# Optimization experiments

Hardware: AMD Instinct MI355X
Metric: run time of the kernel (lower is better)

## Reference

```python
import jax, jax.numpy as jnp
import numpy as np

MARGIN = 1.0
NUM_CLASSES = 1024


def setup_inputs() -> dict:
    key = jax.random.key(0)
    k1, k2 = jax.random.split(key)
    embeddings = jax.random.normal(k1, (8192, 128), dtype=jnp.float32)
    labels = jax.random.randint(k2, (8192,), 0, NUM_CLASSES, dtype=jnp.int64)
    return {"embeddings": embeddings, "labels": labels}


def reference(embeddings, labels):
    """Triplet loss with hard-negative mining, fully vectorized.

    Matches TripletLossWithMining(margin=1.0, mining_strategy='hard'):
      - squared-Euclidean pairwise distance matrix, relu-clamped, zero diagonal
      - for every (anchor i, positive p): hardest negative n* = argmin_{n: label!=label_i} d[i,n]
      - triplet kept iff d[i,n*] < d[i,p]; loss = mean relu(d[i,p] - d[i,n*] + margin)
    """
    B = embeddings.shape[0]
    sq = jnp.sum(embeddings * embeddings, axis=1, keepdims=True)          # [B,1]
    dist = sq + sq.T - 2.0 * (embeddings @ embeddings.T)                   # [B,B]
    dist = jax.nn.relu(dist)
    eye = jnp.eye(B, dtype=bool)
    dist = jnp.where(eye, jnp.zeros((), dist.dtype), dist)                 # fill_diagonal_(0)

    same = labels[:, None] == labels[None, :]                              # [B,B]
    pos_mask = same & ~eye
    neg_mask = ~same
    has_neg = jnp.any(neg_mask, axis=1)                                    # [B]

    # hardest (closest) negative per anchor
    neg_d = jnp.where(neg_mask, dist, jnp.array(jnp.inf, dist.dtype))
    hardest_neg = jnp.min(neg_d, axis=1)                                   # [B]

    # triplet (i,p) is kept iff p is a valid positive, i has a negative,
    # and hardest_neg[i] < pos_dist d[i,p]
    valid = pos_mask & has_neg[:, None] & (hardest_neg[:, None] < dist)    # [B,B]

    per_triplet = jax.nn.relu(dist - hardest_neg[:, None] + MARGIN)        # [B,B]
    count = jnp.sum(valid)
    total = jnp.sum(jnp.where(valid, per_triplet, jnp.zeros((), dist.dtype)))
    loss = total / jnp.maximum(count, 1).astype(dist.dtype)
    return loss, count
```

## Files before the change

kernel.cpp:

```cpp
#include <hip/hip_runtime.h>
#include <stdint.h>

#define BB 8192
#define DD 128
#define MARGIN 1.0f
#define CCAP 48
#define NBLK_POS (BB / 4)
#define NCH 16
#define CHCOLS (BB / NCH)
#define TPC (CHCOLS / 64)

typedef __attribute__((ext_vector_type(8))) short short8_t;
typedef __attribute__((ext_vector_type(4))) float f32x4;

#define GLL16(g, l)                                                                   \
  __builtin_amdgcn_global_load_lds(                                                   \
      (const __attribute__((address_space(1))) unsigned int*)(g),                     \
      (__attribute__((address_space(3))) unsigned int*)(l), 16, 0, 0)

__device__ __forceinline__ unsigned short f2bf(float f) {
  unsigned u = __float_as_uint(f);
  u = (u + 0x7fffu + ((u >> 16) & 1u)) >> 16;
  return (unsigned short)u;
}

__global__ void prep_kernel(const float* __restrict__ E, const int* __restrict__ lab,
                            unsigned short* __restrict__ Ebf,
                            float* __restrict__ sq,
                            int* __restrict__ cls_cnt, int* __restrict__ cls_idx) {
  int wid = threadIdx.x >> 6, lane = threadIdx.x & 63;
  int row = blockIdx.x * 4 + wid;
  const float2 v = *(const float2*)(E + (size_t)row * DD + lane * 2);
  ushort2 bb;
  bb.x = f2bf(v.x);
  bb.y = f2bf(v.y);
  *(ushort2*)(Ebf + (size_t)row * DD + lane * 2) = bb;
  float s = v.x * v.x + v.y * v.y;
  for (int off = 1; off < 64; off <<= 1) s += __shfl_xor(s, off);
  if (lane == 0) {
    sq[row] = s;
    int labi = lab[row];
    int p = atomicAdd(&cls_cnt[labi], 1);
    if (p < CCAP) cls_idx[labi * CCAP + p] = row;
  }
}

__global__ __launch_bounds__(256, 3) void dist_min_kernel(
    const unsigned short* __restrict__ Ebf, const float* __restrict__ sq,
    const int* __restrict__ lab, float* __restrict__ part) {
  __shared__ __align__(16) char ldsB[2][64 * 256];
  __shared__ int labC[CHCOLS];
  __shared__ float hC[CHCOLS];
  __shared__ int labI[128];
  __shared__ float redMin[4][64];

  const int tid = threadIdx.x;
  const int p = blockIdx.x >> 4, c = blockIdx.x & (NCH - 1);
  const int rI = p * 128;
  const int cBase = c * CHCOLS;

  const int wid = tid >> 6, lane = tid & 63;
  const int l4 = lane >> 4, c16 = lane & 15;
  const int wr = wid >> 1, wc = wid & 1;
  const int rowbase = wr * 64;
  const int cl = c16, rg = l4;

  short8_t a[4][4];
#pragma unroll
  for (int m = 0; m < 4; m++) {
    const char* rowp = (const char*)Ebf + (size_t)(rI + rowbase + m * 16 + cl) * 256 + rg * 16;
#pragma unroll
    for (int kk = 0; kk < 4; kk++) a[m][kk] = *(const short8_t*)(rowp + kk * 64);
  }

#pragma unroll
  for (int q = 0; q < 4; q++) {
    int r = wid * 16 + q * 4 + l4;
    int chunk = c16 ^ (r & 7);
    GLL16((const char*)Ebf + (size_t)(cBase + r) * 256 + chunk * 16,
          ldsB[0] + wid * 4096 + q * 1024);
  }
  for (int q = tid; q < CHCOLS; q += 256) {
    labC[q] = lab[cBase + q];
    hC[q] = 0.5f * sq[cBase + q];
  }
  if (tid < 128) labI[tid] = lab[rI + tid];
  __syncthreads();

  int il[4][4];
#pragma unroll
  for (int m = 0; m < 4; m++)
#pragma unroll
    for (int r = 0; r < 4; r++) il[m][r] = labI[rowbase + m * 16 + rg * 4 + r];

  float tm[4][4];
#pragma unroll
  for (int m = 0; m < 4; m++)
#pragma unroll
    for (int r = 0; r < 4; r++) tm[m][r] = __builtin_huge_valf();

  for (int t = 0; t < TPC; t++) {
    const int cur = t & 1;
    if (t + 1 < TPC) {
#pragma unroll
      for (int q = 0; q < 4; q++) {
        int r = wid * 16 + q * 4 + l4;
        int chunk = c16 ^ (r & 7);
        GLL16((const char*)Ebf + (size_t)(cBase + (t + 1) * 64 + r) * 256 + chunk * 16,
              ldsB[cur ^ 1] + wid * 4096 + q * 1024);
      }
    }

    int jl[2];
    float jh[2];
#pragma unroll
    for (int n = 0; n < 2; n++) {
      int j = t * 64 + wc * 32 + n * 16 + cl;
      jl[n] = labC[j];
      jh[n] = hC[j];
    }

    f32x4 acc[4][2];
#pragma unroll
    for (int m = 0; m < 4; m++)
#pragma unroll
      for (int n = 0; n < 2; n++) acc[m][n] = (f32x4){0.f, 0.f, 0.f, 0.f};

#pragma unroll
    for (int kk = 0; kk < 4; kk++) {
      const int kb = kk * 64 + rg * 16;
      short8_t b[2];
#pragma unroll
      for (int n = 0; n < 2; n++) {
        int row = wc * 32 + n * 16 + cl;
        b[n] = *(const short8_t*)(ldsB[cur] + row * 256 + (kb ^ ((row & 7) << 4)));
      }
#pragma unroll
      for (int m = 0; m < 4; m++)
#pragma unroll
        for (int n = 0; n < 2; n++)
          acc[m][n] = __builtin_amdgcn_mfma_f32_16x16x32_bf16(a[m][kk], b[n], acc[m][n], 0, 0, 0);
    }

#pragma unroll
    for (int m = 0; m < 4; m++)
#pragma unroll
      for (int n = 0; n < 2; n++) {
        f32x4 v = acc[m][n];
#pragma unroll
        for (int r = 0; r < 4; r++) {
          float u = jh[n] - v[r];
          if (il[m][r] != jl[n]) tm[m][r] = fminf(tm[m][r], u);
        }
      }

    __syncthreads();
  }

#pragma unroll
  for (int m = 0; m < 4; m++)
#pragma unroll
    for (int r = 0; r < 4; r++) {
      float t = tm[m][r];
      t = fminf(t, __shfl_xor(t, 1));
      t = fminf(t, __shfl_xor(t, 2));
      t = fminf(t, __shfl_xor(t, 4));
      t = fminf(t, __shfl_xor(t, 8));
      tm[m][r] = t;
    }
  if (cl == 0) {
#pragma unroll
    for (int m = 0; m < 4; m++)
#pragma unroll
      for (int r = 0; r < 4; r++) redMin[wid][m * 16 + rg * 4 + r] = tm[m][r];
  }
  __syncthreads();
  if (wc == 0) {
    float v = fminf(redMin[wid][lane], redMin[wid + 1][lane]);
    part[(size_t)c * BB + rI + rowbase + lane] = v;
  }
}

__global__ void pos_loss_kernel(const float* __restrict__ E, const int* __restrict__ lab,
                                const float* __restrict__ sq, const float* __restrict__ part,
                                const int* __restrict__ cls_cnt, const int* __restrict__ cls_idx,
                                float* __restrict__ ptot, int* __restrict__ pcnt) {
  __shared__ float stot[4];
  __shared__ int scnt[4];
  const int tid = threadIdx.x, wid = tid >> 6, lane = tid & 63;
  const int i = blockIdx.x * 4 + wid;
  const int labi = lab[i];
  int n = cls_cnt[labi];
  if (n > CCAP) n = CCAP;
  const float2 ei = *(const float2*)(E + (size_t)i * DD + lane * 2);
  const float sqi = sq[i];
  float mn = __builtin_huge_valf();
#pragma unroll
  for (int cc = 0; cc < NCH; cc++) mn = fminf(mn, part[(size_t)cc * BB + i]);
  const float hn = fmaxf(sqi + 2.0f * mn, 0.0f);
  float tsum = 0.0f;
  int tcnt = 0;
  for (int s = 0; s < n; s++) {
    int j = cls_idx[labi * CCAP + s];
    if (j == i) continue;
    float2 ej = *(const float2*)(E + (size_t)j * DD + lane * 2);
    float pp = ei.x * ej.x + ei.y * ej.y;
    for (int off = 1; off < 64; off <<= 1) pp += __shfl_xor(pp, off);
    float d = fmaxf(sqi + sq[j] - 2.0f * pp, 0.0f);
    if (hn < d) {
      tcnt++;
      tsum += d - hn + MARGIN;
    }
  }
  if (lane == 0) {
    stot[wid] = tsum;
    scnt[wid] = tcnt;
  }
  __syncthreads();
  if (tid == 0) {
    ptot[blockIdx.x] = stot[0] + stot[1] + stot[2] + stot[3];
    pcnt[blockIdx.x] = scnt[0] + scnt[1] + scnt[2] + scnt[3];
  }
}

__global__ void finalize_kernel(const float* __restrict__ ptot, const int* __restrict__ pcnt,
                                float* __restrict__ out) {
  __shared__ float stot[4];
  __shared__ int scnt[4];
  const int tid = threadIdx.x, wid = tid >> 6, lane = tid & 63;
  float t = 0.0f;
  int c = 0;
  for (int k = tid; k < NBLK_POS; k += 256) {
    t += ptot[k];
    c += pcnt[k];
  }
  for (int off = 1; off < 64; off <<= 1) {
    t += __shfl_xor(t, off);
    c += __shfl_xor(c, off);
  }
  if (lane == 0) {
    stot[wid] = t;
    scnt[wid] = c;
  }
  __syncthreads();
  if (tid == 0) {
    float tt = stot[0] + stot[1] + stot[2] + stot[3];
    int cc = scnt[0] + scnt[1] + scnt[2] + scnt[3];
    out[0] = tt / (float)(cc > 0 ? cc : 1);
    out[1] = (float)cc;
  }
}

extern "C" void kernel_launch(void* const* d_in, const int* in_sizes, int n_in,
                              void* d_out, int out_size, void* d_ws, size_t ws_size,
                              hipStream_t stream) {
  const float* E = (const float*)d_in[0];
  const int* lab = (const int*)d_in[1];
  float* out = (float*)d_out;

  char* ws = (char*)d_ws;
  unsigned short* Ebf = (unsigned short*)ws;
  float* sq = (float*)(ws + (size_t)BB * DD * 2);
  int* cls_cnt = (int*)((char*)sq + BB * 4);
  int* cls_idx = (int*)((char*)cls_cnt + 1024 * 4);
  float* ptot = (float*)((char*)cls_idx + 1024 * CCAP * 4);
  int* pcnt = (int*)((char*)ptot + NBLK_POS * 4);
  float* part = (float*)((char*)pcnt + NBLK_POS * 4);

  hipMemsetAsync(cls_cnt, 0, 1024 * 4, stream);
  prep_kernel<<<BB / 4, 256, 0, stream>>>(E, lab, Ebf, sq, cls_cnt, cls_idx);
  dist_min_kernel<<<64 * NCH, 256, 0, stream>>>(Ebf, sq, lab, part);
  pos_loss_kernel<<<NBLK_POS, 256, 0, stream>>>(E, lab, sq, part, cls_cnt, cls_idx, ptot, pcnt);
  finalize_kernel<<<1, 256, 0, stream>>>(ptot, pcnt, out);
}
```

Baseline: 121.8 us.

## Prefetch two tiles ahead with manual waitcnt and fully unroll the tile loop

The dist_min_kernel now issues loads for the first two B tiles up front and fills tile t+2 only after finishing tile t. It replaces __syncthreads with explicit s_waitcnt vmcnt(4) plus raw s_barrier, so one tile's global-to-LDS load stays in flight during compute. The tile loop is fully unrolled and the A fragments are pinned in registers, aiming to hide load latency and barrier cost. The hand-counted vmcnt relies on the compiler's exact load ordering and on the A loads finishing first, and the unrolling raises code size and register pressure.

```diff
diff --git a/kernel.cpp b/kernel.cpp
--- a/kernel.cpp
+++ b/kernel.cpp
@@ -17,6 +17,8 @@
   __builtin_amdgcn_global_load_lds(                                                   \
       (const __attribute__((address_space(1))) unsigned int*)(g),                     \
       (__attribute__((address_space(3))) unsigned int*)(l), 16, 0, 0)
+
+#define KEEP(x) asm volatile("" ::"v"(x))
 
 __device__ __forceinline__ unsigned short f2bf(float f) {
   unsigned u = __float_as_uint(f);
@@ -73,42 +75,52 @@
     for (int kk = 0; kk < 4; kk++) a[m][kk] = *(const short8_t*)(rowp + kk * 64);
   }
 
-#pragma unroll
-  for (int q = 0; q < 4; q++) {
-    int r = wid * 16 + q * 4 + l4;
-    int chunk = c16 ^ (r & 7);
-    GLL16((const char*)Ebf + (size_t)(cBase + r) * 256 + chunk * 16,
-          ldsB[0] + wid * 4096 + q * 1024);
-  }
+#define STAGE_B(tt, buf)                                                            \
+  {                                                                                 \
+    _Pragma("unroll") for (int q = 0; q < 4; q++) {                                 \
+      int r = wid * 16 + q * 4 + l4;                                                \
+      int chunk = c16 ^ (r & 7);                                                    \
+      GLL16((const char*)Ebf + (size_t)(cBase + (tt)*64 + r) * 256 + chunk * 16,    \
+            (buf) + wid * 4096 + q * 1024);                                         \
+    }                                                                               \
+  }
+
+  STAGE_B(0, ldsB[0]);
+  STAGE_B(1, ldsB[1]);
+
   for (int q = tid; q < CHCOLS; q += 256) {
     labC[q] = lab[cBase + q];
     hC[q] = 0.5f * sq[cBase + q];
   }
   if (tid < 128) labI[tid] = lab[rI + tid];
-  __syncthreads();
+
+#pragma unroll
+  for (int m = 0; m < 4; m++)
+#pragma unroll
+    for (int kk = 0; kk < 4; kk++) KEEP(a[m][kk]);
 
   int il[4][4];
+  float tm[4][4];
 #pragma unroll
   for (int m = 0; m < 4; m++)
 #pragma unroll
-    for (int r = 0; r < 4; r++) il[m][r] = labI[rowbase + m * 16 + rg * 4 + r];
-
-  float tm[4][4];
-#pragma unroll
-  for (int m = 0; m < 4; m++)
-#pragma unroll
     for (int r = 0; r < 4; r++) tm[m][r] = __builtin_huge_valf();
 
+#pragma unroll
   for (int t = 0; t < TPC; t++) {
-    const int cur = t & 1;
-    if (t + 1 < TPC) {
-#pragma unroll
-      for (int q = 0; q < 4; q++) {
-        int r = wid * 16 + q * 4 + l4;
-        int chunk = c16 ^ (r & 7);
-        GLL16((const char*)Ebf + (size_t)(cBase + (t + 1) * 64 + r) * 256 + chunk * 16,
-              ldsB[cur ^ 1] + wid * 4096 + q * 1024);
-      }
+    if (t < TPC - 1)
+      asm volatile("s_waitcnt vmcnt(4) lgkmcnt(0)" ::: "memory");
+    else
+      asm volatile("s_waitcnt vmcnt(0) lgkmcnt(0)" ::: "memory");
+    __builtin_amdgcn_sched_barrier(0);
+    __builtin_amdgcn_s_barrier();
+    __builtin_amdgcn_sched_barrier(0);
+
+    if (t == 0) {
+#pragma unroll
+      for (int m = 0; m < 4; m++)
+#pragma unroll
+        for (int r = 0; r < 4; r++) il[m][r] = labI[rowbase + m * 16 + rg * 4 + r];
     }
 
     int jl[2];
@@ -133,7 +145,7 @@
 #pragma unroll
       for (int n = 0; n < 2; n++) {
         int row = wc * 32 + n * 16 + cl;
-        b[n] = *(const short8_t*)(ldsB[cur] + row * 256 + (kb ^ ((row & 7) << 4)));
+        b[n] = *(const short8_t*)(ldsB[t & 1] + row * 256 + (kb ^ ((row & 7) << 4)));
       }
 #pragma unroll
       for (int m = 0; m < 4; m++)
@@ -154,7 +166,9 @@
         }
       }
 
-    __syncthreads();
+    __builtin_amdgcn_s_barrier();
+    __builtin_amdgcn_sched_barrier(0);
+    if (t + 2 < TPC) STAGE_B(t + 2, ldsB[t & 1]);
   }
 
 #pragma unroll
```

Result: slower. 147.9 us (+21.4%).
